# Kernel tuning notes

Measured on AMD Instinct MI355X. Metric: run time of the kernel, lower is better.

The kernel has to match this reference:

```python
import jax, jax.numpy as jnp
import numpy as np

NMS_THRESH = 0.3  # default nms_thresh in DetNet.predict


def setup_inputs() -> dict:
    key = jax.random.key(0)
    k1, k2, k3, k4 = jax.random.split(key, 4)
    W, N = 8, 1024
    det = jax.random.uniform(k1, (W, N, 5), dtype=jnp.float32)          # (conf, cx, cy, w, h) in [0,1)
    offsets = jax.random.uniform(k2, (W, 5), dtype=jnp.float32) * 0.5   # window offset vector (0, left, top, 0, 0)-like
    scales = jax.random.uniform(k3, (W, 5), dtype=jnp.float32) * 0.5 + 0.25  # window scale vector
    b = jax.random.uniform(k4, (W, 4), dtype=jnp.float32)
    # (valid_left, valid_right, valid_top, valid_bottom) with left<right, top<bottom
    bounds = jnp.stack([0.3 * b[:, 0], 0.7 + 0.3 * b[:, 1],
                        0.3 * b[:, 2], 0.7 + 0.3 * b[:, 3]], axis=-1)
    return {"det": det, "offsets": offsets, "scales": scales, "bounds": bounds}


def _pairwise_iou(boxes):
    # boxes: [M,4] in (x1,y1,x2,y2)
    x1, y1, x2, y2 = boxes[:, 0], boxes[:, 1], boxes[:, 2], boxes[:, 3]
    area = jnp.clip(x2 - x1, 0.0) * jnp.clip(y2 - y1, 0.0)              # [M]
    iw = jnp.clip(jnp.minimum(x2[:, None], x2[None, :]) - jnp.maximum(x1[:, None], x1[None, :]), 0.0)
    ih = jnp.clip(jnp.minimum(y2[:, None], y2[None, :]) - jnp.maximum(y1[:, None], y1[None, :]), 0.0)
    inter = iw * ih                                                     # [M,M]
    union = area[:, None] + area[None, :] - inter
    return inter / jnp.maximum(union, 1e-9)


def reference(det, offsets, scales, bounds):
    W, N, _ = det.shape
    M = W * N
    cx, cy = det[..., 1], det[..., 2]                                    # [W,N]
    left, right = bounds[:, 0:1], bounds[:, 1:2]
    top, bottom = bounds[:, 2:3], bounds[:, 3:4]
    valid = (cx < right) & (cx > left) & (cy < bottom) & (cy > top)      # [W,N] border mask
    # torch.addcmul(offset, d, scale) = offset + d * scale
    d = (offsets[:, None, :] + det * scales[:, None, :]).reshape(M, 5)
    valid = valid.reshape(M)
    scores = jnp.where(valid, d[:, 0], -1.0)                             # invalid boxes never kept
    order = jnp.argsort(-scores)                                         # descending confidence
    d_s = d[order]                                                       # [M,5]
    s_s = scores[order]
    # point_form: (cx,cy,w,h) -> (x1,y1,x2,y2)
    cxy, wh = d_s[:, 1:3], d_s[:, 3:5]
    boxes = jnp.concatenate([cxy - wh * 0.5, cxy + wh * 0.5], axis=-1)
    iou = jax.lax.stop_gradient(_pairwise_iou(boxes))                    # [M,M], suppression is non-diff
    s_c = jax.lax.stop_gradient(s_s)
    idx = jnp.arange(M)

    def body(i, keep):
        # suppressed if any kept higher-score box overlaps > thresh
        sup = jnp.any(keep & (idx < i) & (iou[:, i] > NMS_THRESH))
        return keep.at[i].set(jnp.logical_and(~sup, s_c[i] > 0.0))

    keep = jax.lax.fori_loop(0, M, body, jnp.ones((M,), dtype=bool))
    return d_s * keep[:, None].astype(d_s.dtype)                         # [M,5], suppressed rows zeroed
```

## Files before the change

### kernel.cpp

```cpp
#include <hip/hip_runtime.h>
#include <cstdint>


#define M_TOT 8192
#define NMS_T 0.3f
#define PCMAX 24

#define WS_BOX   65536
#define WS_D     196608
#define WS_VCNT  360448
#define WS_ZROW  393216
#define WS_MASK  524288

typedef unsigned long long u64t;

__device__ __forceinline__ uint32_t desc_key(float sv) {
    uint32_t u = __float_as_uint(sv);
    uint32_t m = (u & 0x80000000u) ? ~u : (u | 0x80000000u);
    return ~m;
}
__device__ __forceinline__ u64t rdl64(u64t v, int sl) {
    unsigned lo = (unsigned)__builtin_amdgcn_readlane((int)(unsigned)v, sl);
    unsigned hi = (unsigned)__builtin_amdgcn_readlane((int)(unsigned)(v >> 32), sl);
    return ((u64t)hi << 32) | lo;
}
__device__ __forceinline__ u64t rdfl64(u64t v) {
    unsigned lo = (unsigned)__builtin_amdgcn_readfirstlane((int)(unsigned)v);
    unsigned hi = (unsigned)__builtin_amdgcn_readfirstlane((int)(unsigned)(v >> 32));
    return ((u64t)hi << 32) | lo;
}

__device__ __forceinline__ void scatter_one(
    int i, int rank, u64t key,
    const float* __restrict__ det, const float* __restrict__ offsets,
    const float* __restrict__ scales,
    float4* __restrict__ boxes_srt, float* __restrict__ d_srt)
{
    uint32_t dkey = (uint32_t)(key >> 16);
    if (dkey >= 0x7FFFFFFFu) return;
    int g = i >> 10;
    float d0 = __fadd_rn(offsets[g*5+0], __fmul_rn(det[i*5+0], scales[g*5+0]));
    float d1 = __fadd_rn(offsets[g*5+1], __fmul_rn(det[i*5+1], scales[g*5+1]));
    float d2 = __fadd_rn(offsets[g*5+2], __fmul_rn(det[i*5+2], scales[g*5+2]));
    float d3 = __fadd_rn(offsets[g*5+3], __fmul_rn(det[i*5+3], scales[g*5+3]));
    float d4 = __fadd_rn(offsets[g*5+4], __fmul_rn(det[i*5+4], scales[g*5+4]));
    d_srt[rank*5+0] = d0; d_srt[rank*5+1] = d1; d_srt[rank*5+2] = d2;
    d_srt[rank*5+3] = d3; d_srt[rank*5+4] = d4;
    float hw = __fmul_rn(d3, 0.5f), hh = __fmul_rn(d4, 0.5f);
    boxes_srt[rank] = make_float4(__fsub_rn(d1, hw), __fsub_rn(d2, hh),
                                  __fadd_rn(d1, hw), __fadd_rn(d2, hh));
}

__global__ __launch_bounds__(512) void k2_rank(
    const float* __restrict__ det, const float* __restrict__ offsets,
    const float* __restrict__ scales, const float* __restrict__ bounds,
    float4* __restrict__ boxes_srt, float* __restrict__ d_srt,
    unsigned int* __restrict__ vcnt, u64t* __restrict__ zrow,
    float* __restrict__ out)
{
    __shared__ u64t skey[M_TOT];
    __shared__ float soff[40], sscl[40], sbnd[32];
    __shared__ int sTop;
    int t = threadIdx.x;
    int lane = t & 63;
    if (t == 0) sTop = 0;
    if (t < 40) { soff[t] = offsets[t]; sscl[t] = scales[t]; }
    if (t < 32) { sbnd[t] = bounds[t]; }
    if (blockIdx.x == 0 && t < 128) zrow[t] = 0ull;
    __syncthreads();

    #pragma unroll 4
    for (int s = 0; s < 16; ++s) {
        int u = s * 512 + t;
        int g = u >> 10;
        float raw_s = det[u * 5 + 0];
        float cx    = det[u * 5 + 1];
        float cy    = det[u * 5 + 2];
        float score = __fadd_rn(soff[g * 5 + 0], __fmul_rn(raw_s, sscl[g * 5 + 0]));
        bool valid = (cx < sbnd[g*4+1]) && (cx > sbnd[g*4+0]) &&
                     (cy < sbnd[g*4+3]) && (cy > sbnd[g*4+2]);
        float sv = valid ? score : -1.0f;
        uint32_t dk = desc_key(sv);
        bool push = dk < 0x7FFFFFFFu;
        u64t key = ((u64t)dk << 16) | (unsigned)u;
        u64t bal = __ballot(push);
        if (bal) {
            int lw = 0;
            if (lane == 0) lw = atomicAdd(&sTop, __popcll(bal));
            int wbase = __builtin_amdgcn_readfirstlane(lw);
            if (push) {
                int off = __popcll(bal & ((1ull << lane) - 1ull));
                skey[wbase + off] = key;
            }
        }
    }
    __syncthreads();
    int V = sTop;
    int Vpad = (V + 15) & ~15;
    if (t < Vpad - V) skey[V + t] = ~0ull;
    {
        int zb = blockIdx.x * 320;
        for (int z = zb + t; z < zb + 320; z += 512) out[z] = 0.0f;
    }
    __syncthreads();
    if (t == 0) *vcnt = (unsigned)V;

    int grp = t >> 3;
    int jq  = t & 7;
    int i = blockIdx.x * 64 + grp;
    int g = i >> 10;
    float raw_s = det[i * 5 + 0];
    float cx    = det[i * 5 + 1];
    float cy    = det[i * 5 + 2];
    float score = __fadd_rn(soff[g * 5 + 0], __fmul_rn(raw_s, sscl[g * 5 + 0]));
    bool valid = (cx < sbnd[g*4+1]) && (cx > sbnd[g*4+0]) &&
                 (cy < sbnd[g*4+3]) && (cy > sbnd[g*4+2]);
    float sv = valid ? score : -1.0f;
    uint32_t dk = desc_key(sv);
    u64t ki = ((u64t)dk << 16) | (unsigned)i;
    const ulonglong2* skey2 = (const ulonglong2*)skey;
    int c = 0;
    int nit = Vpad >> 4;
    #pragma unroll 4
    for (int it = 0; it < nit; ++it) {
        ulonglong2 kj = skey2[it * 8 + jq];
        c += (kj.x < ki) + (kj.y < ki);
    }
    c += __shfl_xor(c, 1);
    c += __shfl_xor(c, 2);
    c += __shfl_xor(c, 4);
    if (jq == 0)
        scatter_one(i, c, ki, det, offsets, scales, boxes_srt, d_srt);
}

__global__ __launch_bounds__(256) void k_mask(
    const float4* __restrict__ boxes_srt,
    const unsigned int* __restrict__ vcnt,
    u64t* __restrict__ mask)
{
    __shared__ float4 sb[8 * 65];
    __shared__ float  sa[8 * 65];
    int V = (int)*vcnt;
    int bx = blockIdx.x, by = blockIdx.y;
    if (bx * 32 >= V) return;
    if (by * 512 >= V) return;
    if (by * 8 + 7 < (bx * 32) >> 6) return;
    int nc = (V + 63) >> 6;
    int tid = threadIdx.x;
    int cbase = by * 512;
    for (int u = tid; u < 512; u += 256) {
        float4 b = boxes_srt[cbase + u];
        int c = u >> 6, jj = u & 63;
        sb[c * 65 + jj] = b;
        sa[c * 65 + jj] = __fmul_rn(fmaxf(__fsub_rn(b.z, b.x), 0.0f),
                                    fmaxf(__fsub_rn(b.w, b.y), 0.0f));
    }
    __syncthreads();
    int r = bx * 32 + (tid >> 3);
    if (r >= V) return;
    float4 bi = boxes_srt[r];
    float ai = __fmul_rn(fmaxf(__fsub_rn(bi.z, bi.x), 0.0f),
                         fmaxf(__fsub_rn(bi.w, bi.y), 0.0f));
    int rw = r >> 6;
    int wl = tid & 7;
    int w = by * 8 + wl;
    if (w < rw || w >= nc) return;
    u64t bits = 0;
    #pragma unroll 4
    for (int jj = 0; jj < 64; ++jj) {
        float4 bj = sb[wl * 65 + jj];
        float aj = sa[wl * 65 + jj];
        float iw = fmaxf(__fsub_rn(fminf(bi.z, bj.z), fmaxf(bi.x, bj.x)), 0.0f);
        float ih = fmaxf(__fsub_rn(fminf(bi.w, bj.w), fmaxf(bi.y, bj.y)), 0.0f);
        float inter = __fmul_rn(iw, ih);
        float uni   = __fsub_rn(__fadd_rn(ai, aj), inter);
        float iou   = __fdiv_rn(inter, fmaxf(uni, 1e-9f));
        int j = w * 64 + jj;
        if (j > r && iou > NMS_T) bits |= 1ull << jj;
    }
    mask[(size_t)r * 128 + w] = bits;
}

__global__ __launch_bounds__(512) void k3_serial(
    const u64t* __restrict__ mask, const u64t* __restrict__ zrow,
    const float* __restrict__ d_srt, const unsigned int* __restrict__ vcnt,
    float* __restrict__ out)
{
    __shared__ u64t sband[PCMAX * 128 * 4];
    __shared__ u64t sdead[128];
    __shared__ u64t ck[128];
    __shared__ int  res_prog;
    __shared__ int  h_prog[7];
    int tid = threadIdx.x, wv = tid >> 6, lane = tid & 63;
    int V = (int)*vcnt;
    int nc = (V + 127) >> 7;
    int PC = min(nc, PCMAX);

    if (tid < 128) {
        int bw = tid * 64;
        u64t w0 = 0;
        if (bw >= V)           w0 = ~0ull;
        else if (bw + 64 > V)  w0 = (~0ull) << (V - bw);
        sdead[tid] = w0;
        ck[tid] = 0ull;
    }
    if (tid == 0) res_prog = 0;
    if (tid < 7)  h_prog[tid] = tid;
    for (int e = tid; e < PC * 128; e += 512) {
        int c = e >> 7;
        const u64t* rp = mask + (size_t)e * 128;
        ulonglong2 lo = *(const ulonglong2*)(rp + 2 * c);
        ulonglong2 hi = *(const ulonglong2*)(rp + 2 * c + 2);
        ulonglong2* bp = (ulonglong2*)(sband + (size_t)e * 4);
        bp[0] = lo; bp[1] = hi;
    }
    __syncthreads();

    if (wv == 0) {
        u64t cA_lo = 0, cA_hi = 0;
        for (int T = 0; T < nc; ++T) {
            ulonglong2 bl, bln, bh, bhn;
            if (T < PC) {
                const ulonglong2* p0 = (const ulonglong2*)(sband + (size_t)(T * 128 + lane) * 4);
                const ulonglong2* p1 = (const ulonglong2*)(sband + (size_t)(T * 128 + 64 + lane) * 4);
                bl = p0[0]; bln = p0[1];
                bh = p1[0]; bhn = p1[1];
            } else {
                int rl = min(T * 128 + lane,      M_TOT - 1);
                int rh = min(T * 128 + 64 + lane, M_TOT - 1);
                int w = min(2 * T, 124);
                const u64t* rpl = mask + (size_t)rl * 128;
                const u64t* rph = mask + (size_t)rh * 128;
                bl  = *(const ulonglong2*)(rpl + w);
                bln = *(const ulonglong2*)(rpl + w + 2);
                bh  = *(const ulonglong2*)(rph + w);
                bhn = *(const ulonglong2*)(rph + w + 2);
            }
            if (T >= 2) {
                int need = T - 1;
                while (true) {
                    int hp = (lane < 7) ? ((volatile int*)h_prog)[lane] : 0x7FFFFFFF;
                    if (__ballot(hp < need) == 0ull) break;
                }
            }
            u64t dlo = rdfl64(((volatile u64t*)sdead)[2 * T]);
            u64t dhi = rdfl64(((volatile u64t*)sdead)[2 * T + 1]);
            u64t live_lo = ~(dlo | cA_lo);
            u64t live_hi = ~(dhi | cA_hi);
            int rem = V - T * 128;
            if (rem < 128) {
                live_lo &= (rem >= 64) ? ~0ull : ((rem <= 0) ? 0ull : ((1ull << rem) - 1ull));
                int rh = rem - 64;
                live_hi &= (rh >= 64) ? ~0ull : ((rh <= 0) ? 0ull : ((1ull << rh) - 1ull));
            }
            u64t km_lo = 0, km_hi = 0;
            while (live_lo) {
                int bs = (int)__builtin_ctzll(live_lo);
                km_lo |= 1ull << bs;
                u64t rml = rdl64(bl.x, bs);
                u64t rmh = rdl64(bl.y, bs);
                live_lo &= ~rml & ~(1ull << bs);
                live_hi &= ~rmh;
            }
            while (live_hi) {
                int bs = (int)__builtin_ctzll(live_hi);
                km_hi |= 1ull << bs;
                u64t rmh = rdl64(bh.y, bs);
                live_hi &= ~rmh & ~(1ull << bs);
            }
            if (lane == 0) { ck[2 * T] = km_lo; ck[2 * T + 1] = km_hi; }
            __threadfence_block();
            if (lane == 0) *(volatile int*)&res_prog = T + 1;
            u64t c1l = 0, c1h = 0, km = km_lo;
            while (km) {
                int b = (int)__builtin_ctzll(km); km &= km - 1;
                c1l |= rdl64(bln.x, b); c1h |= rdl64(bln.y, b);
            }
            km = km_hi;
            while (km) {
                int b = (int)__builtin_ctzll(km); km &= km - 1;
                c1l |= rdl64(bhn.x, b); c1h |= rdl64(bhn.y, b);
            }
            cA_lo = c1l; cA_hi = c1h;
        }
    } else {
        int hh = wv - 1;
        for (int c = hh; c < nc; c += 7) {
            while (*(volatile int*)&res_prog <= c) __builtin_amdgcn_s_sleep(1);
            u64t kl = ((volatile u64t*)ck)[2 * c];
            u64t kh = ((volatile u64t*)ck)[2 * c + 1];
            if (kl | kh) {
                int base = c * 128;
                u64t ax = 0, ay = 0;
                while (kl | kh) {
                    ulonglong2 b[4];
                    #pragma unroll
                    for (int q = 0; q < 4; ++q) {
                        const ulonglong2* ptr;
                        if (kl) {
                            int b_ = __builtin_ctzll(kl); kl &= kl - 1;
                            ptr = (const ulonglong2*)(mask + (size_t)(base + b_) * 128) + lane;
                        } else if (kh) {
                            int b_ = __builtin_ctzll(kh); kh &= kh - 1;
                            ptr = (const ulonglong2*)(mask + (size_t)(base + 64 + b_) * 128) + lane;
                        } else {
                            ptr = (const ulonglong2*)zrow + lane;
                        }
                        b[q] = *ptr;
                    }
                    ax |= b[0].x | b[1].x | b[2].x | b[3].x;
                    ay |= b[0].y | b[1].y | b[2].y | b[3].y;
                }
                atomicOr(&sdead[2 * lane],     ax);
                atomicOr(&sdead[2 * lane + 1], ay);
            }
            __threadfence_block();
            if (lane == 0) ((volatile int*)h_prog)[hh] = c + 7;
        }
        if (lane == 0) ((volatile int*)h_prog)[hh] = 0x7FFFFFFF;
    }
    __syncthreads();
    if (tid < 128) {
        u64t m = ck[tid];
        while (m) {
            int b = __builtin_ctzll(m); m &= m - 1;
            int rr = tid * 64 + b;
            out[rr * 5 + 0] = d_srt[rr * 5 + 0];
            out[rr * 5 + 1] = d_srt[rr * 5 + 1];
            out[rr * 5 + 2] = d_srt[rr * 5 + 2];
            out[rr * 5 + 3] = d_srt[rr * 5 + 3];
            out[rr * 5 + 4] = d_srt[rr * 5 + 4];
        }
    }
}

extern "C" void kernel_launch(void* const* d_in, const int* in_sizes, int n_in,
                              void* d_out, int out_size, void* d_ws, size_t ws_size,
                              hipStream_t stream) {
    const float* det     = (const float*)d_in[0];
    const float* offsets = (const float*)d_in[1];
    const float* scales  = (const float*)d_in[2];
    const float* bounds  = (const float*)d_in[3];
    float* out = (float*)d_out;
    char* ws = (char*)d_ws;
    float4*       boxes = (float4*)(ws + WS_BOX);
    float*        d_srt = (float*)(ws + WS_D);
    unsigned int* vcnt  = (unsigned int*)(ws + WS_VCNT);
    u64t*         zrow  = (u64t*)(ws + WS_ZROW);
    u64t*         mask  = (u64t*)(ws + WS_MASK);

    k2_rank<<<128, 512, 0, stream>>>(det, offsets, scales, bounds, boxes, d_srt, vcnt, zrow, out);
    k_mask<<<dim3(256, 16), 256, 0, stream>>>(boxes, vcnt, mask);
    k3_serial<<<1, 512, 0, stream>>>(mask, zrow, d_srt, vcnt, out);
}
```

Before: 138.1 us.

## Fuse IoU mask build and serial NMS with per-chunk completion counters

Merges the mask-computation kernel and the single-block serial suppression kernel into one launch. Block 0 runs the serial scan while 127 worker blocks fill mask tiles chunk by chunk in row order, publishing progress through atomic done counters. The serial wavefront waits on each chunk's counter and prefetches the next chunk's diagonal mask words, so it no longer preloads a band into shared memory. This is meant to overlap mask building with the serial scan and remove a launch gap. In exchange it relies on co-residency of all 128 blocks and adds cross-block spin-waits, and the mask grid shrinks from a 2D launch to 127 workers.

```diff
diff --git a/kernel.cpp b/kernel.cpp
--- a/kernel.cpp
+++ b/kernel.cpp
@@ -4,12 +4,12 @@
 
 #define M_TOT 8192
 #define NMS_T 0.3f
-#define PCMAX 24
 
 #define WS_BOX   65536
 #define WS_D     196608
 #define WS_VCNT  360448
 #define WS_ZROW  393216
+#define WS_DONE  458752
 #define WS_MASK  524288
 
 typedef unsigned long long u64t;
@@ -56,7 +56,7 @@
     const float* __restrict__ scales, const float* __restrict__ bounds,
     float4* __restrict__ boxes_srt, float* __restrict__ d_srt,
     unsigned int* __restrict__ vcnt, u64t* __restrict__ zrow,
-    float* __restrict__ out)
+    unsigned int* __restrict__ done, float* __restrict__ out)
 {
     __shared__ u64t skey[M_TOT];
     __shared__ float soff[40], sscl[40], sbnd[32];
@@ -67,6 +67,7 @@
     if (t < 40) { soff[t] = offsets[t]; sscl[t] = scales[t]; }
     if (t < 32) { sbnd[t] = bounds[t]; }
     if (blockIdx.x == 0 && t < 128) zrow[t] = 0ull;
+    if (blockIdx.x == 0 && t < 64)  done[t] = 0u;
     __syncthreads();
 
     #pragma unroll 4
@@ -133,167 +134,202 @@
         scatter_one(i, c, ki, det, offsets, scales, boxes_srt, d_srt);
 }
 
-__global__ __launch_bounds__(256) void k_mask(
+__global__ __launch_bounds__(512) void k34_fused(
     const float4* __restrict__ boxes_srt,
+    const u64t* __restrict__ zrow,
+    const float* __restrict__ d_srt,
     const unsigned int* __restrict__ vcnt,
-    u64t* __restrict__ mask)
-{
-    __shared__ float4 sb[8 * 65];
-    __shared__ float  sa[8 * 65];
-    int V = (int)*vcnt;
-    int bx = blockIdx.x, by = blockIdx.y;
-    if (bx * 32 >= V) return;
-    if (by * 512 >= V) return;
-    if (by * 8 + 7 < (bx * 32) >> 6) return;
-    int nc = (V + 63) >> 6;
-    int tid = threadIdx.x;
-    int cbase = by * 512;
-    for (int u = tid; u < 512; u += 256) {
-        float4 b = boxes_srt[cbase + u];
-        int c = u >> 6, jj = u & 63;
-        sb[c * 65 + jj] = b;
-        sa[c * 65 + jj] = __fmul_rn(fmaxf(__fsub_rn(b.z, b.x), 0.0f),
-                                    fmaxf(__fsub_rn(b.w, b.y), 0.0f));
-    }
-    __syncthreads();
-    int r = bx * 32 + (tid >> 3);
-    if (r >= V) return;
-    float4 bi = boxes_srt[r];
-    float ai = __fmul_rn(fmaxf(__fsub_rn(bi.z, bi.x), 0.0f),
-                         fmaxf(__fsub_rn(bi.w, bi.y), 0.0f));
-    int rw = r >> 6;
-    int wl = tid & 7;
-    int w = by * 8 + wl;
-    if (w < rw || w >= nc) return;
-    u64t bits = 0;
-    #pragma unroll 4
-    for (int jj = 0; jj < 64; ++jj) {
-        float4 bj = sb[wl * 65 + jj];
-        float aj = sa[wl * 65 + jj];
-        float iw = fmaxf(__fsub_rn(fminf(bi.z, bj.z), fmaxf(bi.x, bj.x)), 0.0f);
-        float ih = fmaxf(__fsub_rn(fminf(bi.w, bj.w), fmaxf(bi.y, bj.y)), 0.0f);
-        float inter = __fmul_rn(iw, ih);
-        float uni   = __fsub_rn(__fadd_rn(ai, aj), inter);
-        float iou   = __fdiv_rn(inter, fmaxf(uni, 1e-9f));
-        int j = w * 64 + jj;
-        if (j > r && iou > NMS_T) bits |= 1ull << jj;
-    }
-    mask[(size_t)r * 128 + w] = bits;
-}
-
-__global__ __launch_bounds__(512) void k3_serial(
-    const u64t* __restrict__ mask, const u64t* __restrict__ zrow,
-    const float* __restrict__ d_srt, const unsigned int* __restrict__ vcnt,
+    u64t* __restrict__ mask,
+    unsigned int* __restrict__ done,
     float* __restrict__ out)
 {
-    __shared__ u64t sband[PCMAX * 128 * 4];
+    int V = (int)*vcnt;
+    int nwords = (V + 63) >> 6;
+    int nc = (V + 127) >> 7;
+    int tid = threadIdx.x;
+
+    if (blockIdx.x != 0) {
+        __shared__ float4 sb[8 * 65];
+        __shared__ float  sa[8 * 65];
+        int b = (int)blockIdx.x - 1;
+        int gpre = 0;
+        for (int c = 0; c < nc; ++c) {
+            int w0 = 2 * c;
+            int Wc = nwords - w0;
+            int tiles = 2 * ((Wc + 7) >> 3);
+            int tau0 = ((b - gpre) % 127 + 127) % 127;
+            for (int tau = tau0; tau < tiles; tau += 127) {
+                int rt = tau & 1, wt = tau >> 1;
+                int rowbase = c * 128 + rt * 64;
+                int wbase = w0 + wt * 8;
+                {
+                    int u = tid;
+                    float4 bb = boxes_srt[min(wbase * 64 + u, M_TOT - 1)];
+                    int cc = u >> 6, jj = u & 63;
+                    sb[cc * 65 + jj] = bb;
+                    sa[cc * 65 + jj] = __fmul_rn(fmaxf(__fsub_rn(bb.z, bb.x), 0.0f),
+                                                 fmaxf(__fsub_rn(bb.w, bb.y), 0.0f));
+                }
+                __syncthreads();
+                int r  = rowbase + (tid >> 3);
+                int wl = tid & 7;
+                int w  = wbase + wl;
+                if (r < V && w < nwords) {
+                    float4 bi = boxes_srt[r];
+                    float ai = __fmul_rn(fmaxf(__fsub_rn(bi.z, bi.x), 0.0f),
+                                         fmaxf(__fsub_rn(bi.w, bi.y), 0.0f));
+                    u64t bits = 0;
+                    #pragma unroll 4
+                    for (int jj = 0; jj < 64; ++jj) {
+                        float4 bj = sb[wl * 65 + jj];
+                        float aj = sa[wl * 65 + jj];
+                        float iw = fmaxf(__fsub_rn(fminf(bi.z, bj.z), fmaxf(bi.x, bj.x)), 0.0f);
+                        float ih = fmaxf(__fsub_rn(fminf(bi.w, bj.w), fmaxf(bi.y, bj.y)), 0.0f);
+                        float inter = __fmul_rn(iw, ih);
+                        float uni   = __fsub_rn(__fadd_rn(ai, aj), inter);
+                        float iou   = __fdiv_rn(inter, fmaxf(uni, 1e-9f));
+                        int j = w * 64 + jj;
+                        if (j > r && iou > NMS_T) bits |= 1ull << jj;
+                    }
+                    mask[(size_t)r * 128 + w] = bits;
+                }
+                __syncthreads();
+                if (tid == 0) {
+                    int rows_t  = V - rowbase; if (rows_t > 64) rows_t = 64;
+                    int words_t = nwords - wbase; if (words_t > 8) words_t = 8;
+                    if (rows_t > 0) {
+                        __threadfence();
+                        __hip_atomic_fetch_add(&done[c], (unsigned)(rows_t * words_t),
+                                               __ATOMIC_RELEASE, __HIP_MEMORY_SCOPE_AGENT);
+                    }
+                }
+                __syncthreads();
+            }
+            gpre += tiles;
+        }
+        return;
+    }
+
     __shared__ u64t sdead[128];
     __shared__ u64t ck[128];
     __shared__ int  res_prog;
     __shared__ int  h_prog[7];
-    int tid = threadIdx.x, wv = tid >> 6, lane = tid & 63;
-    int V = (int)*vcnt;
-    int nc = (V + 127) >> 7;
-    int PC = min(nc, PCMAX);
+    int wv = tid >> 6, lane = tid & 63;
 
     if (tid < 128) {
         int bw = tid * 64;
-        u64t w0 = 0;
-        if (bw >= V)           w0 = ~0ull;
-        else if (bw + 64 > V)  w0 = (~0ull) << (V - bw);
-        sdead[tid] = w0;
+        u64t w0v = 0;
+        if (bw >= V)           w0v = ~0ull;
+        else if (bw + 64 > V)  w0v = (~0ull) << (V - bw);
+        sdead[tid] = w0v;
         ck[tid] = 0ull;
     }
     if (tid == 0) res_prog = 0;
     if (tid < 7)  h_prog[tid] = tid;
-    for (int e = tid; e < PC * 128; e += 512) {
-        int c = e >> 7;
-        const u64t* rp = mask + (size_t)e * 128;
-        ulonglong2 lo = *(const ulonglong2*)(rp + 2 * c);
-        ulonglong2 hi = *(const ulonglong2*)(rp + 2 * c + 2);
-        ulonglong2* bp = (ulonglong2*)(sband + (size_t)e * 4);
-        bp[0] = lo; bp[1] = hi;
-    }
     __syncthreads();
 
     if (wv == 0) {
-        u64t cA_lo = 0, cA_hi = 0;
-        for (int T = 0; T < nc; ++T) {
+        if (nc > 0) {
+            u64t cA_lo = 0, cA_hi = 0;
+            {
+                int rows_c = V; if (rows_c > 128) rows_c = 128;
+                unsigned expc = (unsigned)(rows_c * nwords);
+                while (__hip_atomic_load(&done[0], __ATOMIC_RELAXED, __HIP_MEMORY_SCOPE_AGENT) < expc)
+                    __builtin_amdgcn_s_sleep(2);
+                (void)__hip_atomic_load(&done[0], __ATOMIC_ACQUIRE, __HIP_MEMORY_SCOPE_AGENT);
+            }
             ulonglong2 bl, bln, bh, bhn;
-            if (T < PC) {
-                const ulonglong2* p0 = (const ulonglong2*)(sband + (size_t)(T * 128 + lane) * 4);
-                const ulonglong2* p1 = (const ulonglong2*)(sband + (size_t)(T * 128 + 64 + lane) * 4);
-                bl = p0[0]; bln = p0[1];
-                bh = p1[0]; bhn = p1[1];
-            } else {
-                int rl = min(T * 128 + lane,      M_TOT - 1);
-                int rh = min(T * 128 + 64 + lane, M_TOT - 1);
-                int w = min(2 * T, 124);
+            {
+                int rl = min(lane,      M_TOT - 1);
+                int rh = min(64 + lane, M_TOT - 1);
                 const u64t* rpl = mask + (size_t)rl * 128;
                 const u64t* rph = mask + (size_t)rh * 128;
-                bl  = *(const ulonglong2*)(rpl + w);
-                bln = *(const ulonglong2*)(rpl + w + 2);
-                bh  = *(const ulonglong2*)(rph + w);
-                bhn = *(const ulonglong2*)(rph + w + 2);
-            }
-            if (T >= 2) {
-                int need = T - 1;
-                while (true) {
-                    int hp = (lane < 7) ? ((volatile int*)h_prog)[lane] : 0x7FFFFFFF;
-                    if (__ballot(hp < need) == 0ull) break;
-                }
-            }
-            u64t dlo = rdfl64(((volatile u64t*)sdead)[2 * T]);
-            u64t dhi = rdfl64(((volatile u64t*)sdead)[2 * T + 1]);
-            u64t live_lo = ~(dlo | cA_lo);
-            u64t live_hi = ~(dhi | cA_hi);
-            int rem = V - T * 128;
-            if (rem < 128) {
-                live_lo &= (rem >= 64) ? ~0ull : ((rem <= 0) ? 0ull : ((1ull << rem) - 1ull));
-                int rh = rem - 64;
-                live_hi &= (rh >= 64) ? ~0ull : ((rh <= 0) ? 0ull : ((1ull << rh) - 1ull));
-            }
-            u64t km_lo = 0, km_hi = 0;
-            while (live_lo) {
-                int bs = (int)__builtin_ctzll(live_lo);
-                km_lo |= 1ull << bs;
-                u64t rml = rdl64(bl.x, bs);
-                u64t rmh = rdl64(bl.y, bs);
-                live_lo &= ~rml & ~(1ull << bs);
-                live_hi &= ~rmh;
-            }
-            while (live_hi) {
-                int bs = (int)__builtin_ctzll(live_hi);
-                km_hi |= 1ull << bs;
-                u64t rmh = rdl64(bh.y, bs);
-                live_hi &= ~rmh & ~(1ull << bs);
-            }
-            if (lane == 0) { ck[2 * T] = km_lo; ck[2 * T + 1] = km_hi; }
-            __threadfence_block();
-            if (lane == 0) *(volatile int*)&res_prog = T + 1;
-            u64t c1l = 0, c1h = 0, km = km_lo;
-            while (km) {
-                int b = (int)__builtin_ctzll(km); km &= km - 1;
-                c1l |= rdl64(bln.x, b); c1h |= rdl64(bln.y, b);
-            }
-            km = km_hi;
-            while (km) {
-                int b = (int)__builtin_ctzll(km); km &= km - 1;
-                c1l |= rdl64(bhn.x, b); c1h |= rdl64(bhn.y, b);
-            }
-            cA_lo = c1l; cA_hi = c1h;
+                bl  = *(const ulonglong2*)(rpl);
+                bln = *(const ulonglong2*)(rpl + 2);
+                bh  = *(const ulonglong2*)(rph);
+                bhn = *(const ulonglong2*)(rph + 2);
+            }
+            for (int T = 0; T < nc; ++T) {
+                ulonglong2 nbl, nbln, nbh, nbhn;
+                bool havenext = (T + 1 < nc);
+                if (havenext) {
+                    int c = T + 1;
+                    int rows_c = V - c * 128; if (rows_c > 128) rows_c = 128;
+                    unsigned expc = (unsigned)(rows_c * (nwords - 2 * c));
+                    while (__hip_atomic_load(&done[c], __ATOMIC_RELAXED, __HIP_MEMORY_SCOPE_AGENT) < expc)
+                        __builtin_amdgcn_s_sleep(2);
+                    (void)__hip_atomic_load(&done[c], __ATOMIC_ACQUIRE, __HIP_MEMORY_SCOPE_AGENT);
+                    int rl = min(c * 128 + lane,      M_TOT - 1);
+                    int rh = min(c * 128 + 64 + lane, M_TOT - 1);
+                    int w = min(2 * c, 124);
+                    const u64t* rpl = mask + (size_t)rl * 128;
+                    const u64t* rph = mask + (size_t)rh * 128;
+                    nbl  = *(const ulonglong2*)(rpl + w);
+                    nbln = *(const ulonglong2*)(rpl + w + 2);
+                    nbh  = *(const ulonglong2*)(rph + w);
+                    nbhn = *(const ulonglong2*)(rph + w + 2);
+                }
+                if (T >= 2) {
+                    int need = T - 1;
+                    while (true) {
+                        int hp = (lane < 7) ? ((volatile int*)h_prog)[lane] : 0x7FFFFFFF;
+                        if (__ballot(hp < need) == 0ull) break;
+                    }
+                }
+                u64t dlo = rdfl64(((volatile u64t*)sdead)[2 * T]);
+                u64t dhi = rdfl64(((volatile u64t*)sdead)[2 * T + 1]);
+                u64t live_lo = ~(dlo | cA_lo);
+                u64t live_hi = ~(dhi | cA_hi);
+                int rem = V - T * 128;
+                if (rem < 128) {
+                    live_lo &= (rem >= 64) ? ~0ull : ((rem <= 0) ? 0ull : ((1ull << rem) - 1ull));
+                    int rh = rem - 64;
+                    live_hi &= (rh >= 64) ? ~0ull : ((rh <= 0) ? 0ull : ((1ull << rh) - 1ull));
+                }
+                u64t km_lo = 0, km_hi = 0;
+                while (live_lo) {
+                    int bs = (int)__builtin_ctzll(live_lo);
+                    km_lo |= 1ull << bs;
+                    u64t rml = rdl64(bl.x, bs);
+                    u64t rmh = rdl64(bl.y, bs);
+                    live_lo &= ~rml & ~(1ull << bs);
+                    live_hi &= ~rmh;
+                }
+                while (live_hi) {
+                    int bs = (int)__builtin_ctzll(live_hi);
+                    km_hi |= 1ull << bs;
+                    u64t rmh = rdl64(bh.y, bs);
+                    live_hi &= ~rmh & ~(1ull << bs);
+                }
+                if (lane == 0) { ck[2 * T] = km_lo; ck[2 * T + 1] = km_hi; }
+                __threadfence_block();
+                if (lane == 0) *(volatile int*)&res_prog = T + 1;
+                u64t c1l = 0, c1h = 0, km = km_lo;
+                while (km) {
+                    int b_ = (int)__builtin_ctzll(km); km &= km - 1;
+                    c1l |= rdl64(bln.x, b_); c1h |= rdl64(bln.y, b_);
+                }
+                km = km_hi;
+                while (km) {
+                    int b_ = (int)__builtin_ctzll(km); km &= km - 1;
+                    c1l |= rdl64(bhn.x, b_); c1h |= rdl64(bhn.y, b_);
+                }
+                cA_lo = c1l; cA_hi = c1h;
+                if (havenext) { bl = nbl; bln = nbln; bh = nbh; bhn = nbhn; }
+            }
         }
     } else {
         int hh = wv - 1;
         for (int c = hh; c < nc; c += 7) {
             while (*(volatile int*)&res_prog <= c) __builtin_amdgcn_s_sleep(1);
+            (void)__hip_atomic_load(&done[c], __ATOMIC_ACQUIRE, __HIP_MEMORY_SCOPE_AGENT);
             u64t kl = ((volatile u64t*)ck)[2 * c];
             u64t kh = ((volatile u64t*)ck)[2 * c + 1];
             if (kl | kh) {
                 int base = c * 128;
                 u64t ax = 0, ay = 0;
                 while (kl | kh) {
-                    ulonglong2 b[4];
+                    ulonglong2 bq[4];
                     #pragma unroll
                     for (int q = 0; q < 4; ++q) {
                         const ulonglong2* ptr;
@@ -306,10 +342,10 @@
                         } else {
                             ptr = (const ulonglong2*)zrow + lane;
                         }
-                        b[q] = *ptr;
+                        bq[q] = *ptr;
                     }
-                    ax |= b[0].x | b[1].x | b[2].x | b[3].x;
-                    ay |= b[0].y | b[1].y | b[2].y | b[3].y;
+                    ax |= bq[0].x | bq[1].x | bq[2].x | bq[3].x;
+                    ay |= bq[0].y | bq[1].y | bq[2].y | bq[3].y;
                 }
                 atomicOr(&sdead[2 * lane],     ax);
                 atomicOr(&sdead[2 * lane + 1], ay);
@@ -323,8 +359,8 @@
     if (tid < 128) {
         u64t m = ck[tid];
         while (m) {
-            int b = __builtin_ctzll(m); m &= m - 1;
-            int rr = tid * 64 + b;
+            int b_ = __builtin_ctzll(m); m &= m - 1;
+            int rr = tid * 64 + b_;
             out[rr * 5 + 0] = d_srt[rr * 5 + 0];
             out[rr * 5 + 1] = d_srt[rr * 5 + 1];
             out[rr * 5 + 2] = d_srt[rr * 5 + 2];
@@ -347,9 +383,9 @@
     float*        d_srt = (float*)(ws + WS_D);
     unsigned int* vcnt  = (unsigned int*)(ws + WS_VCNT);
     u64t*         zrow  = (u64t*)(ws + WS_ZROW);
+    unsigned int* done  = (unsigned int*)(ws + WS_DONE);
     u64t*         mask  = (u64t*)(ws + WS_MASK);
 
-    k2_rank<<<128, 512, 0, stream>>>(det, offsets, scales, bounds, boxes, d_srt, vcnt, zrow, out);
-    k_mask<<<dim3(256, 16), 256, 0, stream>>>(boxes, vcnt, mask);
-    k3_serial<<<1, 512, 0, stream>>>(mask, zrow, d_srt, vcnt, out);
-}
+    k2_rank<<<128, 512, 0, stream>>>(det, offsets, scales, bounds, boxes, d_srt, vcnt, zrow, done, out);
+    k34_fused<<<128, 512, 0, stream>>>(boxes, zrow, d_srt, vcnt, mask, done, out);
+}
```

After: 138.7 us. Within noise of the previous version (+0.4%).
